# Performance work log

Hardware: AMD Instinct MI355X
Metric: run time of the kernel (lower is better)

Reference implementation:

```python
import jax, jax.numpy as jnp
import numpy as np

HEADS = 8
B, N, DIM = 8, 1024, 128  # n must be a perfect square (H=W=32)
LN_EPS = 1e-5


def _region_means(xg):
    """Four-quadrant region means per position via integral image.
    xg: [b,H,W,d] -> [b,H,W,4,d]. For position (h,w) the torch code pools:
      r1 = x[:, :h+1, :w+1], r2 = x[:, :h+1, w:], r3 = x[:, h:, :w+1], r4 = x[:, h:, w:]
    """
    b, H, W, d = xg.shape
    # padded 2D prefix sum: P[:, i, j] = sum over rows<i, cols<j
    P = jnp.pad(jnp.cumsum(jnp.cumsum(xg, axis=1), axis=2),
                ((0, 0), (1, 0), (1, 0), (0, 0)))
    r1 = P[:, 1:, 1:]                                              # sum x[:h+1,:w+1]
    r2 = P[:, 1:, -1:] - P[:, 1:, :-1]                             # sum x[:h+1, w:]
    r3 = P[:, -1:, 1:] - P[:, :-1, 1:]                             # sum x[h:, :w+1]
    r4 = P[:, -1:, -1:] - P[:, :-1, -1:] - P[:, -1:, :-1] + P[:, :-1, :-1]
    ah = jnp.arange(H, dtype=xg.dtype)
    aw = jnp.arange(W, dtype=xg.dtype)
    hp1 = (ah + 1.0)[:, None]   # h+1
    wp1 = (aw + 1.0)[None, :]   # w+1
    hr = (H - ah)[:, None]      # H-h
    wr = (W - aw)[None, :]      # W-w
    c1 = (hp1 * wp1)[None, :, :, None]
    c2 = (hp1 * wr)[None, :, :, None]
    c3 = (hr * wp1)[None, :, :, None]
    c4 = (hr * wr)[None, :, :, None]
    return jnp.stack([r1 / c1, r2 / c2, r3 / c3, r4 / c4], axis=3)


def setup_inputs() -> dict:
    key = jax.random.key(0)
    ks = jax.random.split(key, 10)
    s = 0.02
    return {
        "x": jax.random.normal(ks[0], (B, N, DIM), jnp.float32),
        "ln_g": jnp.ones((DIM,), jnp.float32),
        "ln_b": jnp.zeros((DIM,), jnp.float32),
        "Wqkv": jax.random.normal(ks[1], (DIM, 3 * HEADS * DIM), jnp.float32) * s,
        "bqkv": jax.random.normal(ks[2], (3 * HEADS * DIM,), jnp.float32) * s,
        "Wq": jax.random.normal(ks[3], (DIM, DIM), jnp.float32) * s,
        "Wk": jax.random.normal(ks[4], (DIM, DIM), jnp.float32) * s,
        "Wv": jax.random.normal(ks[5], (DIM, DIM), jnp.float32) * s,
        "Wo": jax.random.normal(ks[6], (DIM, DIM), jnp.float32) * s,
        "bo": jax.random.normal(ks[7], (DIM,), jnp.float32) * s,
        "Wout": jax.random.normal(ks[8], (HEADS * DIM, DIM), jnp.float32) * s,
        "bout": jax.random.normal(ks[9], (DIM,), jnp.float32) * s,
    }


def reference(x, ln_g, ln_b, Wqkv, bqkv, Wq, Wk, Wv, Wo, bo, Wout, bout):
    b, n, dim = x.shape
    H = W = int(n ** 0.5)
    # LayerNorm
    mu = jnp.mean(x, axis=-1, keepdims=True)
    var = jnp.mean(jnp.square(x - mu), axis=-1, keepdims=True)
    xn = (x - mu) * jax.lax.rsqrt(var + LN_EPS) * ln_g + ln_b
    # qkv projection; only q is actually used downstream (k,v chunks are dead)
    qkv = xn @ Wqkv + bqkv
    q = qkv[..., : HEADS * dim].reshape(b, n, HEADS, dim).transpose(0, 2, 1, 3)  # [b,h,n,d]
    # region features, identical across heads -> keep unbroadcast [b,n,4,d]
    regions = _region_means(xn.reshape(b, H, W, dim)).reshape(b, n, 4, dim)
    # RegionAggregator
    qh = q @ Wq                                   # [b,h,n,d]
    k = jnp.einsum('bnrd,de->bnre', regions, Wk)  # [b,n,4,d]
    v = jnp.einsum('bnrd,de->bnre', regions, Wv)
    scale = (dim // HEADS) ** -0.5
    attn = jax.nn.softmax(jnp.einsum('bhnd,bnrd->bhnr', qh, k) * scale, axis=-1)
    agg = jnp.einsum('bhnr,bnrd->bhnd', attn, v)
    out = agg @ Wo + bo                           # [b,h,n,d]
    out = out.transpose(0, 2, 1, 3).reshape(b, n, HEADS * dim)
    return out @ Wout + bout
```

## Files before the change

### kernel.cpp

```cpp
#include <hip/hip_runtime.h>
#include <hip/hip_bf16.h>
#include <stdint.h>

#define HEADS 8
#define NN 1024
#define DIM 128
#define HW 32
#define LN_EPS 1e-5f

typedef __hip_bfloat16 bf16;
typedef __bf16 bf16x8 __attribute__((ext_vector_type(8)));
typedef float floatx4 __attribute__((ext_vector_type(4)));

__device__ __forceinline__ float b2f(bf16 v){ return __bfloat162float(v); }
__device__ __forceinline__ bf16 f2b(float v){ return __float2bfloat16(v); }

__device__ __forceinline__ float ldin(const void* p, size_t i, int f){
    return f ? ((const float*)p)[i] : b2f(((const bf16*)p)[i]);
}
__device__ __forceinline__ float4 ldin4(const void* p, size_t i, int f){
    if (f) return *reinterpret_cast<const float4*>((const float*)p + i);
    ushort4 u = *reinterpret_cast<const ushort4*>((const bf16*)p + i);
    float4 r;
    r.x = b2f(*(bf16*)&u.x); r.y = b2f(*(bf16*)&u.y);
    r.z = b2f(*(bf16*)&u.z); r.w = b2f(*(bf16*)&u.w);
    return r;
}
__device__ __forceinline__ int dtf(const void* g){
    return (((const uint32_t*)g)[0] == 0x3F800000u) ? 1 : 0;
}

__global__ __launch_bounds__(1024) void lnscan_kernel(const void* __restrict__ x,
                                                      const void* __restrict__ g,
                                                      const void* __restrict__ bta,
                                                      bf16* __restrict__ xn,
                                                      float* __restrict__ P){
    __shared__ float lnv[32][128];
    int f = dtf(g);
    int b = blockIdx.x >> 5, hh = blockIdx.x & 31;
    int wv = threadIdx.x >> 6, lane = threadIdx.x & 63;
    float gl0 = ldin(g, lane, f),    gl1 = ldin(g, lane+64, f);
    float bl0 = ldin(bta, lane, f),  bl1 = ldin(bta, lane+64, f);
    size_t rowbase = (size_t)b*NN + (size_t)hh*HW;
#pragma unroll
    for (int rnd=0; rnd<2; rnd++){
        int w = rnd*16 + wv;
        size_t base = (rowbase + w)*DIM;
        float v0 = ldin(x, base+lane,    f);
        float v1 = ldin(x, base+lane+64, f);
        float s = v0+v1, ss = v0*v0+v1*v1;
        for (int o=32;o;o>>=1){ s += __shfl_xor(s,o,64); ss += __shfl_xor(ss,o,64); }
        float mu = s * (1.0f/DIM);
        float var = ss * (1.0f/DIM) - mu*mu;
        float rs = rsqrtf(var + LN_EPS);
        float y0 = (v0-mu)*rs*gl0 + bl0;
        float y1 = (v1-mu)*rs*gl1 + bl1;
        xn[base+lane]    = f2b(y0);
        xn[base+lane+64] = f2b(y1);
        lnv[w][lane]    = y0;
        lnv[w][lane+64] = y1;
    }
    __syncthreads();
    if (threadIdx.x < 128){
        int c = threadIdx.x;
        float run = 0.f;
        float* Pr = P + rowbase*DIM + c;
#pragma unroll
        for (int w=0; w<HW; w++){
            run += lnv[w][c];
            Pr[(size_t)w*DIM] = run;
        }
    }
}

__global__ __launch_bounds__(128) void colscan_kernel(float* __restrict__ P){
    int b = blockIdx.x >> 5, w = blockIdx.x & 31, c = threadIdx.x;
    float* Pc = P + ((size_t)(b*NN + w))*DIM + c;
    float run = 0.f;
    for (int h=0; h<HW; h++){
        size_t o = (size_t)h*HW*DIM;
        run += Pc[o]; Pc[o] = run;
    }
}

__global__ __launch_bounds__(256) void prep_kernel(const void* __restrict__ Wqkv,
                                                   const void* __restrict__ bqkv,
                                                   const void* __restrict__ Wq,
                                                   const void* __restrict__ Wk,
                                                   const void* __restrict__ Wv,
                                                   const void* __restrict__ Wo,
                                                   const void* __restrict__ bo,
                                                   const void* __restrict__ Wout,
                                                   const void* __restrict__ ln_g,
                                                   bf16* __restrict__ WhT,
                                                   bf16* __restrict__ WhoT,
                                                   bf16* __restrict__ WkvT,
                                                   float* __restrict__ bq,
                                                   float* __restrict__ bfin_part){
    __shared__ float S1[128][132];
    __shared__ float S2[8][132];
    int f = dtf(ln_g);
    int t = threadIdx.x;
    int blk = blockIdx.x;
    if (blk < 128){
        int h = blk >> 4, dc = blk & 15;
#pragma unroll
        for (int i=0;i<16;i++){
            int idx4 = (t + i*256)*4;
            int k = idx4 >> 7, e = idx4 & 127;
            *reinterpret_cast<float4*>(&S1[k][e]) = ldin4(Wq, idx4, f);
        }
        {
            int idx4 = t*4;
            int dl = idx4 >> 7, k = idx4 & 127;
            *reinterpret_cast<float4*>(&S2[dl][k]) =
                ldin4(Wqkv, (size_t)(dc*8+dl)*3072 + h*128 + k, f);
        }
        __syncthreads();
        int d = t & 7;
        int e0 = (t >> 3) * 4;
        float acc[4] = {0.f,0.f,0.f,0.f};
        for (int k=0;k<128;k++){
            float a = S2[d][k];
            float4 wv = *reinterpret_cast<const float4*>(&S1[k][e0]);
            acc[0] += a*wv.x; acc[1] += a*wv.y; acc[2] += a*wv.z; acc[3] += a*wv.w;
        }
#pragma unroll
        for (int i=0;i<4;i++)
            WhT[(size_t)(h*128 + e0 + i)*128 + dc*8 + d] = f2b(acc[i]);
    } else if (blk < 256){
        int h = (blk-128) >> 4, dc = (blk-128) & 15;
#pragma unroll
        for (int i=0;i<16;i++){
            int idx4 = (t + i*256)*4;
            int k = idx4 >> 7, e = idx4 & 127;
            *reinterpret_cast<float4*>(&S1[k][e]) =
                ldin4(Wout, (size_t)(h*128 + k)*128 + e, f);
        }
        {
            int idx4 = t*4;
            int dl = idx4 >> 7, k = idx4 & 127;
            *reinterpret_cast<float4*>(&S2[dl][k]) =
                ldin4(Wo, (size_t)(dc*8+dl)*128 + k, f);
        }
        __syncthreads();
        int d = t & 7;
        int e0 = (t >> 3) * 4;
        float acc[4] = {0.f,0.f,0.f,0.f};
        for (int k=0;k<128;k++){
            float a = S2[d][k];
            float4 wv = *reinterpret_cast<const float4*>(&S1[k][e0]);
            acc[0] += a*wv.x; acc[1] += a*wv.y; acc[2] += a*wv.z; acc[3] += a*wv.w;
        }
#pragma unroll
        for (int i=0;i<4;i++)
            WhoT[(size_t)(e0 + i)*1024 + h*128 + dc*8 + d] = f2b(acc[i]);
    } else {
        int sub = blk - 256;
        if (sub < 8){
            int h = sub;
            int e = t & 127, kh = t >> 7;
            float s = 0.f;
            for (int k=kh*64; k<kh*64+64; k++)
                s += ldin(bqkv, h*128 + k, f) * ldin(Wq, (size_t)k*128 + e, f);
            S1[kh][e] = s;
            __syncthreads();
            if (t < 128) bq[h*128 + t] = S1[0][t] + S1[1][t];
        } else if (sub < 16){
            int h = sub - 8;
            if (t < 128) S2[0][t] = ldin(bo, t, f);
            __syncthreads();
            int e = t & 127, half = t >> 7;
            float s = 0.f;
            for (int k = half*64; k < half*64 + 64; k++)
                s += S2[0][k] * ldin(Wout, (size_t)(h*128 + k)*128 + e, f);
            S1[half][e] = s;
            __syncthreads();
            if (t < 128) bfin_part[h*128 + t] = S1[0][t] + S1[1][t];
        } else {
            const void* W = (sub == 16) ? Wk : Wv;
            int base = (sub == 16) ? 0 : 128;
#pragma unroll
            for (int i=0;i<16;i++){
                int idx4 = (t + i*256)*4;
                int d = idx4 >> 7, e = idx4 & 127;
                *reinterpret_cast<float4*>(&S1[d][e]) = ldin4(W, idx4, f);
            }
            __syncthreads();
            for (int i=0;i<64;i++){
                int idx = t + i*256; int e = idx >> 7, d = idx & 127;
                WkvT[(size_t)(base + e)*128 + d] = f2b(S1[d][e]);
            }
        }
    }
}

__global__ __launch_bounds__(512, 2) void attn_fused_kernel(const float* __restrict__ P,
                                                            const bf16* __restrict__ WkvT,
                                                            const bf16* __restrict__ WhT,
                                                            const bf16* __restrict__ WhoT,
                                                            const float* __restrict__ bq,
                                                            const float* __restrict__ bfin_part,
                                                            const void* __restrict__ bout,
                                                            const bf16* __restrict__ xn,
                                                            const void* __restrict__ ln_g,
                                                            void* __restrict__ out){
    __shared__ __align__(16) char pool[60800];
    bf16 (*As)[136]     = reinterpret_cast<bf16(*)[136]>(pool);
    bf16 (*vS)[16][136] = reinterpret_cast<bf16(*)[16][136]>(pool);
    bf16 (*kS)[16][136] = reinterpret_cast<bf16(*)[16][136]>(pool + 17408);
    bf16 (*qL)[16][136] = reinterpret_cast<bf16(*)[16][136]>(pool + 34816);
    bf16 (*xnS)[136]    = reinterpret_cast<bf16(*)[136]>(pool + 52224);
    float* logits       = reinterpret_cast<float*>(pool + 56576);
    float* pp           = reinterpret_cast<float*>(pool + 58624);

    int f = dtf(ln_g);
    int t = threadIdx.x;
    int bn0 = blockIdx.x * 16;
    {
        int bn_local = t >> 5;
        int c0 = (t & 31) * 4;
        int bn = bn0 + bn_local;
        int b = bn >> 10, n = bn & 1023;
        int hh = n >> 5, ww = n & 31;
        const float* Pb = P + (size_t)b*NN*DIM;
        auto ld4 = [&](int h, int w, float* o){
            if (h==0 || w==0){ o[0]=o[1]=o[2]=o[3]=0.f; return; }
            const float* p = Pb + ((size_t)((h-1)*HW + (w-1)))*DIM + c0;
            float4 u = *reinterpret_cast<const float4*>(p);
            o[0]=u.x;o[1]=u.y;o[2]=u.z;o[3]=u.w;
        };
        float f_h1 = (float)(hh+1), f_w1 = (float)(ww+1);
        float f_hr = (float)(HW-hh), f_wr = (float)(HW-ww);
        float a0[4], a1[4], a2[4], a3[4];
        ld4(hh+1, ww+1, a0);
#pragma unroll
        for (int j=0;j<4;j++) As[bn_local*4 + 0][c0+j] = f2b(a0[j] / (f_h1*f_w1));
        ld4(hh+1, HW, a0); ld4(hh+1, ww, a1);
#pragma unroll
        for (int j=0;j<4;j++) As[bn_local*4 + 1][c0+j] = f2b((a0[j]-a1[j]) / (f_h1*f_wr));
        ld4(HW, ww+1, a0); ld4(hh, ww+1, a1);
#pragma unroll
        for (int j=0;j<4;j++) As[bn_local*4 + 2][c0+j] = f2b((a0[j]-a1[j]) / (f_hr*f_w1));
        ld4(HW, HW, a0); ld4(hh, HW, a1); ld4(HW, ww, a2); ld4(hh, ww, a3);
#pragma unroll
        for (int j=0;j<4;j++)
            As[bn_local*4 + 3][c0+j] = f2b((a0[j]-a1[j]-a2[j]+a3[j]) / (f_hr*f_wr));
        *reinterpret_cast<uint2*>(&xnS[bn_local][c0]) =
            *reinterpret_cast<const uint2*>(&xn[(size_t)(bn0 + bn_local)*DIM + c0]);
    }
    int w = t >> 6, lane = t & 63;
    int r = lane & 15, q = lane >> 4;
    int mh = w & 3, nh = w >> 2;
    __syncthreads();
    floatx4 acc[4];
#pragma unroll
    for (int i=0;i<4;i++) acc[i] = (floatx4){0.f,0.f,0.f,0.f};
#pragma unroll
    for (int kc=0;kc<4;kc++){
        bf16x8 a = *reinterpret_cast<const bf16x8*>(&As[mh*16 + r][kc*32 + q*8]);
#pragma unroll
        for (int nt=0;nt<4;nt++){
            bf16x8 b = *reinterpret_cast<const bf16x8*>(
                &WkvT[(size_t)(nh*64 + nt*16 + r)*128 + kc*32 + q*8]);
            acc[nt] = __builtin_amdgcn_mfma_f32_16x16x32_bf16(a, b, acc[nt], 0, 0, 0);
        }
    }
#pragma unroll
    for (int nt=0;nt<4;nt++)
#pragma unroll
        for (int i=0;i<4;i++){
            int rowg = mh*16 + q*4 + i;
            kS[rowg & 3][rowg >> 2][nh*64 + nt*16 + r] = f2b(acc[nt][i]);
        }
#pragma unroll
    for (int i=0;i<4;i++) acc[i] = (floatx4){0.f,0.f,0.f,0.f};
#pragma unroll
    for (int kc=0;kc<4;kc++){
        bf16x8 a = *reinterpret_cast<const bf16x8*>(&As[mh*16 + r][kc*32 + q*8]);
#pragma unroll
        for (int nt=0;nt<4;nt++){
            bf16x8 b = *reinterpret_cast<const bf16x8*>(
                &WkvT[(size_t)(128 + nh*64 + nt*16 + r)*128 + kc*32 + q*8]);
            acc[nt] = __builtin_amdgcn_mfma_f32_16x16x32_bf16(a, b, acc[nt], 0, 0, 0);
        }
    }
    __syncthreads();
#pragma unroll
    for (int nt=0;nt<4;nt++)
#pragma unroll
        for (int i=0;i<4;i++){
            int rowg = mh*16 + q*4 + i;
            vS[rowg & 3][rowg >> 2][nh*64 + nt*16 + r] = f2b(acc[nt][i]);
        }
    int rgA = w >> 2, rgB = rgA + 2;
    int hl = w & 3;
    int hq = w >> 1, nl = w & 1;
    for (int g=0; g<2; g++){
        floatx4 qa[4];
#pragma unroll
        for (int i=0;i<4;i++) qa[i] = (floatx4){0.f,0.f,0.f,0.f};
#pragma unroll
        for (int kc=0;kc<4;kc++){
            bf16x8 a = *reinterpret_cast<const bf16x8*>(&xnS[r][kc*32 + q*8]);
#pragma unroll
            for (int nt=0;nt<4;nt++){
                int e = nl*64 + nt*16 + r;
                bf16x8 b = *reinterpret_cast<const bf16x8*>(
                    &WhT[((size_t)((g*4 + hq)*128 + e))*128 + kc*32 + q*8]);
                qa[nt] = __builtin_amdgcn_mfma_f32_16x16x32_bf16(a, b, qa[nt], 0, 0, 0);
            }
        }
        __syncthreads();
#pragma unroll
        for (int nt=0;nt<4;nt++){
            int col = nl*64 + nt*16 + r;
            float bb = bq[(g*4 + hq)*128 + col];
#pragma unroll
            for (int i=0;i<4;i++)
                qL[hq][q*4 + i][col] = f2b(qa[nt][i] + bb);
        }
        __syncthreads();
        {
            floatx4 sA = (floatx4){0.f,0.f,0.f,0.f};
            floatx4 sB = (floatx4){0.f,0.f,0.f,0.f};
#pragma unroll
            for (int kc=0;kc<4;kc++){
                bf16x8 a  = *reinterpret_cast<const bf16x8*>(&qL[hl][r][kc*32 + q*8]);
                bf16x8 kA = *reinterpret_cast<const bf16x8*>(&kS[rgA][r][kc*32 + q*8]);
                bf16x8 kB = *reinterpret_cast<const bf16x8*>(&kS[rgB][r][kc*32 + q*8]);
                sA = __builtin_amdgcn_mfma_f32_16x16x32_bf16(a, kA, sA, 0, 0, 0);
                sB = __builtin_amdgcn_mfma_f32_16x16x32_bf16(a, kB, sB, 0, 0, 0);
            }
            if ((r >> 2) == q){
                int i = r & 3;
                float dA = (i==0)?sA[0]:(i==1)?sA[1]:(i==2)?sA[2]:sA[3];
                float dB = (i==0)?sB[0]:(i==1)?sB[1]:(i==2)?sB[2]:sB[3];
                logits[(r*8 + g*4 + hl)*4 + rgA] = dA;
                logits[(r*8 + g*4 + hl)*4 + rgB] = dB;
            }
        }
    }
    __syncthreads();
    if (t < 128){
        int bn = t >> 3, h = t & 7;
        const float* L = &logits[(bn*8 + h)*4];
        float l0 = L[0]*0.25f, l1 = L[1]*0.25f, l2 = L[2]*0.25f, l3 = L[3]*0.25f;
        float m = fmaxf(fmaxf(l0,l1),fmaxf(l2,l3));
        float e0 = __expf(l0-m), e1=__expf(l1-m), e2=__expf(l2-m), e3=__expf(l3-m);
        float inv = 1.0f/(e0+e1+e2+e3);
        pp[0*136 + h*17 + bn] = e0*inv;
        pp[1*136 + h*17 + bn] = e1*inv;
        pp[2*136 + h*17 + bn] = e2*inv;
        pp[3*136 + h*17 + bn] = e3*inv;
    }
    __syncthreads();
    float4 pv[8];
#pragma unroll
    for (int h=0;h<8;h++){
        pv[h].x = pp[0*136 + h*17 + r];
        pv[h].y = pp[1*136 + h*17 + r];
        pv[h].z = pp[2*136 + h*17 + r];
        pv[h].w = pp[3*136 + h*17 + r];
    }
    floatx4 oacc = (floatx4){0.f,0.f,0.f,0.f};
#pragma unroll
    for (int kc=0;kc<4;kc++){
        int c = kc*32 + q*8;
        bf16x8 v0 = *reinterpret_cast<const bf16x8*>(&vS[0][r][c]);
        bf16x8 v1 = *reinterpret_cast<const bf16x8*>(&vS[1][r][c]);
        bf16x8 v2 = *reinterpret_cast<const bf16x8*>(&vS[2][r][c]);
        bf16x8 v3 = *reinterpret_cast<const bf16x8*>(&vS[3][r][c]);
#pragma unroll
        for (int h=0; h<8; h++){
            bf16x8 a;
#pragma unroll
            for (int j=0;j<8;j++){
                float s = pv[h].x*(float)v0[j] + pv[h].y*(float)v1[j]
                        + pv[h].z*(float)v2[j] + pv[h].w*(float)v3[j];
                a[j] = (__bf16)s;
            }
            bf16x8 b = *reinterpret_cast<const bf16x8*>(
                &WhoT[(size_t)(w*16 + r)*1024 + h*128 + kc*32 + q*8]);
            oacc = __builtin_amdgcn_mfma_f32_16x16x32_bf16(a, b, oacc, 0, 0, 0);
        }
    }
    {
        int col = w*16 + r;
        float bias = ldin(bout, col, f);
#pragma unroll
        for (int h=0;h<8;h++) bias += bfin_part[h*128 + col];
#pragma unroll
        for (int i=0;i<4;i++){
            int row = bn0 + q*4 + i;
            float v = oacc[i] + bias;
            if (f) ((float*)out)[(size_t)row*DIM + col] = v;
            else   ((bf16*)out)[(size_t)row*DIM + col] = f2b(v);
        }
    }
}

extern "C" void kernel_launch(void* const* d_in, const int* in_sizes, int n_in,
                              void* d_out, int out_size, void* d_ws, size_t ws_size,
                              hipStream_t stream){
    const void* x    = d_in[0];
    const void* ln_g = d_in[1];
    const void* ln_b = d_in[2];
    const void* Wqkv = d_in[3];
    const void* bqkv = d_in[4];
    const void* Wq   = d_in[5];
    const void* Wk   = d_in[6];
    const void* Wv   = d_in[7];
    const void* Wo   = d_in[8];
    const void* bo   = d_in[9];
    const void* Wout = d_in[10];
    const void* bout = d_in[11];

    char* ws = (char*)d_ws;
    size_t off = 0;
    auto alloc = [&](size_t bytes)->char*{
        char* p = ws + off; off += (bytes + 255) & ~size_t(255); return p;
    };
    bf16*  WhT   = (bf16*)alloc((size_t)1024*128*2);
    bf16*  WkvT  = (bf16*)alloc((size_t)256*128*2);
    bf16*  WhoT  = (bf16*)alloc((size_t)128*1024*2);
    float* bq    = (float*)alloc(1024*4);
    float* bfin_part = (float*)alloc(8*128*4);
    float* P     = (float*)alloc((size_t)8*NN*DIM*4);
    bf16*  xn    = (bf16*)alloc((size_t)8192*128*2);

    prep_kernel<<<274, 256, 0, stream>>>(Wqkv, bqkv, Wq, Wk, Wv, Wo, bo, Wout,
                                         ln_g, WhT, WhoT, WkvT, bq, bfin_part);
    lnscan_kernel<<<256, 1024, 0, stream>>>(x, ln_g, ln_b, xn, P);
    colscan_kernel<<<256, 128, 0, stream>>>(P);
    attn_fused_kernel<<<512, 512, 0, stream>>>(P, WkvT, WhT, WhoT, bq, bfin_part,
                                               bout, xn, ln_g, d_out);
}
```

Baseline: 150.1 us.

## Halve positions per block in fused attention kernel to double grid size

The fused region-attention kernel now handles 8 positions per block with 256 threads instead of 16 with 512, launching 1024 blocks and halving shared memory so more blocks can be resident per CU. Warp-to-work mappings are reworked: each warp computes a full head's q projection and all four region logits, and the output projection covers two column tiles per warp. MFMA 16-row tiles are now half-filled (rows masked via r&7 and q<2), which wastes matrix throughput and reloads the weights twice as often across blocks, in exchange for better occupancy and load balance.

```diff
diff --git a/kernel.cpp b/kernel.cpp
--- a/kernel.cpp
+++ b/kernel.cpp
@@ -195,7 +195,7 @@
     }
 }
 
-__global__ __launch_bounds__(512, 2) void attn_fused_kernel(const float* __restrict__ P,
+__global__ __launch_bounds__(256, 4) void attn_fused_kernel(const float* __restrict__ P,
                                                             const bf16* __restrict__ WkvT,
                                                             const bf16* __restrict__ WhT,
                                                             const bf16* __restrict__ WhoT,
@@ -205,18 +205,18 @@
                                                             const bf16* __restrict__ xn,
                                                             const void* __restrict__ ln_g,
                                                             void* __restrict__ out){
-    __shared__ __align__(16) char pool[60800];
-    bf16 (*As)[136]     = reinterpret_cast<bf16(*)[136]>(pool);
-    bf16 (*vS)[16][136] = reinterpret_cast<bf16(*)[16][136]>(pool);
-    bf16 (*kS)[16][136] = reinterpret_cast<bf16(*)[16][136]>(pool + 17408);
-    bf16 (*qL)[16][136] = reinterpret_cast<bf16(*)[16][136]>(pool + 34816);
-    bf16 (*xnS)[136]    = reinterpret_cast<bf16(*)[136]>(pool + 52224);
-    float* logits       = reinterpret_cast<float*>(pool + 56576);
-    float* pp           = reinterpret_cast<float*>(pool + 58624);
+    __shared__ __align__(16) char pool[30464];
+    bf16 (*As)[136]    = reinterpret_cast<bf16(*)[136]>(pool);
+    bf16 (*qL)[8][136] = reinterpret_cast<bf16(*)[8][136]>(pool);
+    bf16 (*kS)[8][136] = reinterpret_cast<bf16(*)[8][136]>(pool + 8704);
+    bf16 (*vS)[8][136] = reinterpret_cast<bf16(*)[8][136]>(pool + 17408);
+    bf16 (*xnS)[136]   = reinterpret_cast<bf16(*)[136]>(pool + 26112);
+    float* logits      = reinterpret_cast<float*>(pool + 28288);
+    float* pp          = reinterpret_cast<float*>(pool + 29312);
 
     int f = dtf(ln_g);
     int t = threadIdx.x;
-    int bn0 = blockIdx.x * 16;
+    int bn0 = blockIdx.x * 8;
     {
         int bn_local = t >> 5;
         int c0 = (t & 31) * 4;
@@ -246,12 +246,15 @@
 #pragma unroll
         for (int j=0;j<4;j++)
             As[bn_local*4 + 3][c0+j] = f2b((a0[j]-a1[j]-a2[j]+a3[j]) / (f_hr*f_wr));
-        *reinterpret_cast<uint2*>(&xnS[bn_local][c0]) =
-            *reinterpret_cast<const uint2*>(&xn[(size_t)(bn0 + bn_local)*DIM + c0]);
+        if (t < 128){
+            int row = t >> 4, c8 = t & 15;
+            *reinterpret_cast<uint4*>(&xnS[row][c8*8]) =
+                *reinterpret_cast<const uint4*>(&xn[(size_t)(bn0 + row)*DIM + c8*8]);
+        }
     }
     int w = t >> 6, lane = t & 63;
     int r = lane & 15, q = lane >> 4;
-    int mh = w & 3, nh = w >> 2;
+    int mh = w & 1, nh = w >> 1;
     __syncthreads();
     floatx4 acc[4];
 #pragma unroll
@@ -285,7 +288,6 @@
             acc[nt] = __builtin_amdgcn_mfma_f32_16x16x32_bf16(a, b, acc[nt], 0, 0, 0);
         }
     }
-    __syncthreads();
 #pragma unroll
     for (int nt=0;nt<4;nt++)
 #pragma unroll
@@ -293,84 +295,93 @@
             int rowg = mh*16 + q*4 + i;
             vS[rowg & 3][rowg >> 2][nh*64 + nt*16 + r] = f2b(acc[nt][i]);
         }
-    int rgA = w >> 2, rgB = rgA + 2;
-    int hl = w & 3;
-    int hq = w >> 1, nl = w & 1;
+    __syncthreads();
     for (int g=0; g<2; g++){
-        floatx4 qa[4];
-#pragma unroll
-        for (int i=0;i<4;i++) qa[i] = (floatx4){0.f,0.f,0.f,0.f};
+        int h = g*4 + w;
+        floatx4 qa[8];
+#pragma unroll
+        for (int i=0;i<8;i++) qa[i] = (floatx4){0.f,0.f,0.f,0.f};
 #pragma unroll
         for (int kc=0;kc<4;kc++){
-            bf16x8 a = *reinterpret_cast<const bf16x8*>(&xnS[r][kc*32 + q*8]);
-#pragma unroll
-            for (int nt=0;nt<4;nt++){
-                int e = nl*64 + nt*16 + r;
+            bf16x8 a = *reinterpret_cast<const bf16x8*>(&xnS[r & 7][kc*32 + q*8]);
+#pragma unroll
+            for (int nt=0;nt<8;nt++){
                 bf16x8 b = *reinterpret_cast<const bf16x8*>(
-                    &WhT[((size_t)((g*4 + hq)*128 + e))*128 + kc*32 + q*8]);
+                    &WhT[((size_t)(h*128 + nt*16 + r))*128 + kc*32 + q*8]);
                 qa[nt] = __builtin_amdgcn_mfma_f32_16x16x32_bf16(a, b, qa[nt], 0, 0, 0);
             }
         }
         __syncthreads();
-#pragma unroll
-        for (int nt=0;nt<4;nt++){
-            int col = nl*64 + nt*16 + r;
-            float bb = bq[(g*4 + hq)*128 + col];
-#pragma unroll
-            for (int i=0;i<4;i++)
-                qL[hq][q*4 + i][col] = f2b(qa[nt][i] + bb);
+        if (q < 2){
+#pragma unroll
+            for (int nt=0;nt<8;nt++){
+                int col = nt*16 + r;
+                float bb = bq[h*128 + col];
+#pragma unroll
+                for (int i=0;i<4;i++)
+                    qL[w][q*4 + i][col] = f2b(qa[nt][i] + bb);
+            }
         }
         __syncthreads();
         {
-            floatx4 sA = (floatx4){0.f,0.f,0.f,0.f};
-            floatx4 sB = (floatx4){0.f,0.f,0.f,0.f};
+            floatx4 s0 = (floatx4){0,0,0,0}, s1 = (floatx4){0,0,0,0};
+            floatx4 s2 = (floatx4){0,0,0,0}, s3 = (floatx4){0,0,0,0};
 #pragma unroll
             for (int kc=0;kc<4;kc++){
-                bf16x8 a  = *reinterpret_cast<const bf16x8*>(&qL[hl][r][kc*32 + q*8]);
-                bf16x8 kA = *reinterpret_cast<const bf16x8*>(&kS[rgA][r][kc*32 + q*8]);
-                bf16x8 kB = *reinterpret_cast<const bf16x8*>(&kS[rgB][r][kc*32 + q*8]);
-                sA = __builtin_amdgcn_mfma_f32_16x16x32_bf16(a, kA, sA, 0, 0, 0);
-                sB = __builtin_amdgcn_mfma_f32_16x16x32_bf16(a, kB, sB, 0, 0, 0);
-            }
-            if ((r >> 2) == q){
+                bf16x8 a  = *reinterpret_cast<const bf16x8*>(&qL[w][r & 7][kc*32 + q*8]);
+                bf16x8 k0 = *reinterpret_cast<const bf16x8*>(&kS[0][r & 7][kc*32 + q*8]);
+                bf16x8 k1 = *reinterpret_cast<const bf16x8*>(&kS[1][r & 7][kc*32 + q*8]);
+                bf16x8 k2 = *reinterpret_cast<const bf16x8*>(&kS[2][r & 7][kc*32 + q*8]);
+                bf16x8 k3 = *reinterpret_cast<const bf16x8*>(&kS[3][r & 7][kc*32 + q*8]);
+                s0 = __builtin_amdgcn_mfma_f32_16x16x32_bf16(a, k0, s0, 0, 0, 0);
+                s1 = __builtin_amdgcn_mfma_f32_16x16x32_bf16(a, k1, s1, 0, 0, 0);
+                s2 = __builtin_amdgcn_mfma_f32_16x16x32_bf16(a, k2, s2, 0, 0, 0);
+                s3 = __builtin_amdgcn_mfma_f32_16x16x32_bf16(a, k3, s3, 0, 0, 0);
+            }
+            if ((r >> 2) == q && r < 8){
                 int i = r & 3;
-                float dA = (i==0)?sA[0]:(i==1)?sA[1]:(i==2)?sA[2]:sA[3];
-                float dB = (i==0)?sB[0]:(i==1)?sB[1]:(i==2)?sB[2]:sB[3];
-                logits[(r*8 + g*4 + hl)*4 + rgA] = dA;
-                logits[(r*8 + g*4 + hl)*4 + rgB] = dB;
+                float d0 = (i==0)?s0[0]:(i==1)?s0[1]:(i==2)?s0[2]:s0[3];
+                float d1 = (i==0)?s1[0]:(i==1)?s1[1]:(i==2)?s1[2]:s1[3];
+                float d2 = (i==0)?s2[0]:(i==1)?s2[1]:(i==2)?s2[2]:s2[3];
+                float d3 = (i==0)?s3[0]:(i==1)?s3[1]:(i==2)?s3[2]:s3[3];
+                float* L = &logits[(r*8 + h)*4];
+                L[0] = d0; L[1] = d1; L[2] = d2; L[3] = d3;
             }
         }
     }
     __syncthreads();
-    if (t < 128){
+    if (t < 64){
         int bn = t >> 3, h = t & 7;
         const float* L = &logits[(bn*8 + h)*4];
         float l0 = L[0]*0.25f, l1 = L[1]*0.25f, l2 = L[2]*0.25f, l3 = L[3]*0.25f;
         float m = fmaxf(fmaxf(l0,l1),fmaxf(l2,l3));
         float e0 = __expf(l0-m), e1=__expf(l1-m), e2=__expf(l2-m), e3=__expf(l3-m);
         float inv = 1.0f/(e0+e1+e2+e3);
-        pp[0*136 + h*17 + bn] = e0*inv;
-        pp[1*136 + h*17 + bn] = e1*inv;
-        pp[2*136 + h*17 + bn] = e2*inv;
-        pp[3*136 + h*17 + bn] = e3*inv;
+        pp[0*72 + h*9 + bn] = e0*inv;
+        pp[1*72 + h*9 + bn] = e1*inv;
+        pp[2*72 + h*9 + bn] = e2*inv;
+        pp[3*72 + h*9 + bn] = e3*inv;
     }
     __syncthreads();
     float4 pv[8];
 #pragma unroll
     for (int h=0;h<8;h++){
-        pv[h].x = pp[0*136 + h*17 + r];
-        pv[h].y = pp[1*136 + h*17 + r];
-        pv[h].z = pp[2*136 + h*17 + r];
-        pv[h].w = pp[3*136 + h*17 + r];
-    }
-    floatx4 oacc = (floatx4){0.f,0.f,0.f,0.f};
+        int bnl = r & 7;
+        pv[h].x = pp[0*72 + h*9 + bnl];
+        pv[h].y = pp[1*72 + h*9 + bnl];
+        pv[h].z = pp[2*72 + h*9 + bnl];
+        pv[h].w = pp[3*72 + h*9 + bnl];
+    }
+    floatx4 oacc[2];
+    oacc[0] = (floatx4){0.f,0.f,0.f,0.f};
+    oacc[1] = (floatx4){0.f,0.f,0.f,0.f};
 #pragma unroll
     for (int kc=0;kc<4;kc++){
         int c = kc*32 + q*8;
-        bf16x8 v0 = *reinterpret_cast<const bf16x8*>(&vS[0][r][c]);
-        bf16x8 v1 = *reinterpret_cast<const bf16x8*>(&vS[1][r][c]);
-        bf16x8 v2 = *reinterpret_cast<const bf16x8*>(&vS[2][r][c]);
-        bf16x8 v3 = *reinterpret_cast<const bf16x8*>(&vS[3][r][c]);
+        bf16x8 v0 = *reinterpret_cast<const bf16x8*>(&vS[0][r & 7][c]);
+        bf16x8 v1 = *reinterpret_cast<const bf16x8*>(&vS[1][r & 7][c]);
+        bf16x8 v2 = *reinterpret_cast<const bf16x8*>(&vS[2][r & 7][c]);
+        bf16x8 v3 = *reinterpret_cast<const bf16x8*>(&vS[3][r & 7][c]);
 #pragma unroll
         for (int h=0; h<8; h++){
             bf16x8 a;
@@ -380,22 +391,29 @@
                         + pv[h].z*(float)v2[j] + pv[h].w*(float)v3[j];
                 a[j] = (__bf16)s;
             }
-            bf16x8 b = *reinterpret_cast<const bf16x8*>(
-                &WhoT[(size_t)(w*16 + r)*1024 + h*128 + kc*32 + q*8]);
-            oacc = __builtin_amdgcn_mfma_f32_16x16x32_bf16(a, b, oacc, 0, 0, 0);
-        }
-    }
-    {
-        int col = w*16 + r;
-        float bias = ldin(bout, col, f);
-#pragma unroll
-        for (int h=0;h<8;h++) bias += bfin_part[h*128 + col];
-#pragma unroll
-        for (int i=0;i<4;i++){
-            int row = bn0 + q*4 + i;
-            float v = oacc[i] + bias;
-            if (f) ((float*)out)[(size_t)row*DIM + col] = v;
-            else   ((bf16*)out)[(size_t)row*DIM + col] = f2b(v);
+#pragma unroll
+            for (int nt=0;nt<2;nt++){
+                int ct = w + nt*4;
+                bf16x8 b = *reinterpret_cast<const bf16x8*>(
+                    &WhoT[(size_t)(ct*16 + r)*1024 + h*128 + kc*32 + q*8]);
+                oacc[nt] = __builtin_amdgcn_mfma_f32_16x16x32_bf16(a, b, oacc[nt], 0, 0, 0);
+            }
+        }
+    }
+    if (q < 2){
+#pragma unroll
+        for (int nt=0;nt<2;nt++){
+            int col = (w + nt*4)*16 + r;
+            float bias = ldin(bout, col, f);
+#pragma unroll
+            for (int h=0;h<8;h++) bias += bfin_part[h*128 + col];
+#pragma unroll
+            for (int i=0;i<4;i++){
+                int row = bn0 + q*4 + i;
+                float v = oacc[nt][i] + bias;
+                if (f) ((float*)out)[(size_t)row*DIM + col] = v;
+                else   ((bf16*)out)[(size_t)row*DIM + col] = f2b(v);
+            }
         }
     }
 }
@@ -433,6 +451,6 @@
                                          ln_g, WhT, WhoT, WkvT, bq, bfin_part);
     lnscan_kernel<<<256, 1024, 0, stream>>>(x, ln_g, ln_b, xn, P);
     colscan_kernel<<<256, 128, 0, stream>>>(P);
-    attn_fused_kernel<<<512, 512, 0, stream>>>(P, WkvT, WhT, WhoT, bq, bfin_part,
-                                               bout, xn, ln_g, d_out);
-}
+    attn_fused_kernel<<<1024, 256, 0, stream>>>(P, WkvT, WhT, WhoT, bq, bfin_part,
+                                                bout, xn, ln_g, d_out);
+}
```

Result: slower. 170.0 us (+13.3%).
